# Optimization experiments

Hardware: AMD Instinct MI355X
Metric: run time of the kernel (lower is better)

Reference implementation:

```python
import jax, jax.numpy as jnp
import numpy as np

N_NODES = 50000
N_EDGES = 400000
F_DIM = 128        # num_embeddings
N_TYPES = 100      # num_atoms (embedding vocab)
CUTOFF = 5.0       # cutoff_dist
N_RBF = 20


def setup_inputs() -> dict:
    key = jax.random.key(0)
    ks = jax.random.split(key, 10)
    pos = jax.random.normal(ks[0], (N_NODES, 3), jnp.float32) * 3.0
    z = jax.random.randint(ks[1], (N_NODES,), 0, N_TYPES)
    edge_src = jax.random.randint(ks[2], (N_EDGES,), 0, N_NODES)
    edge_dst = jax.random.randint(ks[3], (N_EDGES,), 0, N_NODES)
    # avoid self-edges (rel_pos = 0 would make RBF sin(x)/x -> nan)
    edge_dst = jnp.where(edge_src == edge_dst, (edge_dst + 1) % N_NODES, edge_dst)
    eq = jnp.zeros((N_NODES, F_DIM, 3), jnp.float32)  # equivariant_repr init
    s = 1.0 / np.sqrt(F_DIM)
    emb_table = jax.random.normal(ks[4], (N_TYPES, F_DIM), jnp.float32) * s
    w_phi1 = jax.random.normal(ks[5], (F_DIM, F_DIM), jnp.float32) * s
    b_phi1 = jnp.zeros((F_DIM,), jnp.float32)
    w_phi2 = jax.random.normal(ks[6], (F_DIM, 3 * F_DIM), jnp.float32) * s
    b_phi2 = jnp.zeros((3 * F_DIM,), jnp.float32)
    w_rbf = jax.random.normal(ks[7], (N_RBF, 3 * F_DIM), jnp.float32) * (1.0 / np.sqrt(N_RBF))
    b_rbf = jnp.zeros((3 * F_DIM,), jnp.float32)
    return {"pos": pos, "eq": eq, "emb_table": emb_table,
            "w_phi1": w_phi1, "b_phi1": b_phi1,
            "w_phi2": w_phi2, "b_phi2": b_phi2,
            "w_rbf": w_rbf, "b_rbf": b_rbf,
            "z": z, "edge_src": edge_src, "edge_dst": edge_dst}


def reference(pos, eq, emb_table, w_phi1, b_phi1, w_phi2, b_phi2, w_rbf, b_rbf,
              z, edge_src, edge_dst):
    N = pos.shape[0]
    F_ = emb_table.shape[1]
    emb = emb_table[z]                                  # [N, F]
    # message pass over all edges (j = src neighbour, i = dst receiving node)
    rel = pos[edge_dst] - pos[edge_src]                 # pos[i] - pos[j], [E, 3]
    dist = jnp.linalg.norm(rel, axis=1)                 # [E]
    n = jnp.arange(1, N_RBF + 1, dtype=pos.dtype)       # [20]
    rbf = jnp.sin(n[None, :] * jnp.pi * dist[:, None] / CUTOFF) / dist[:, None]  # [E, 20]
    phi = jax.nn.silu(emb[edge_src] @ w_phi1 + b_phi1) @ w_phi2 + b_phi2          # [E, 3F]
    W = rbf @ w_rbf + b_rbf                             # [E, 3F]
    split = phi * W                                     # [E, 3F]
    d_emb = jax.ops.segment_sum(split[:, :F_], edge_dst, num_segments=N)          # [N, F]
    eq_msg = (eq[edge_src] * split[:, F_:2 * F_, None]
              + split[:, 2 * F_:, None] * rel[:, None, :] * dist[:, None, None])  # [E, F, 3]
    d_eq = jax.ops.segment_sum(eq_msg, edge_dst, num_segments=N)                  # [N, F, 3]
    return emb + d_emb, eq + d_eq
```

## Files before the change

### kernel.cpp

```cpp
#include <hip/hip_runtime.h>
#include <math.h>

#define N_NODES 50000
#define N_EDGES 400000
#define F_DIM   128
#define N_RBF   20
#define SCAN_B  256
#define N_CHUNK ((N_NODES + SCAN_B - 1) / SCAN_B)

__global__ void phi_table_kernel(const float* __restrict__ emb_table,
                                 const float* __restrict__ w_phi1,
                                 const float* __restrict__ b_phi1,
                                 const float* __restrict__ w_phi2,
                                 const float* __restrict__ b_phi2,
                                 float* __restrict__ phi_table) {
    __shared__ float emb_s[F_DIM];
    __shared__ float h_s[F_DIM];
    const int t = blockIdx.x;
    const int o = threadIdx.x;
    if (o < F_DIM) emb_s[o] = emb_table[t * F_DIM + o];
    __syncthreads();
    if (o < F_DIM) {
        float acc = b_phi1[o];
#pragma unroll 8
        for (int k = 0; k < F_DIM; ++k)
            acc = fmaf(emb_s[k], w_phi1[k * F_DIM + o], acc);
        h_s[o] = acc / (1.0f + expf(-acc));
    }
    __syncthreads();
    float a2 = b_phi2[o];
#pragma unroll 8
    for (int k = 0; k < F_DIM; ++k)
        a2 = fmaf(h_s[k], w_phi2[k * (3 * F_DIM) + o], a2);
    phi_table[t * (3 * F_DIM) + o] = a2;
}

__global__ void count_kernel(const int* __restrict__ edst, int* __restrict__ counts) {
    const int e = blockIdx.x * blockDim.x + threadIdx.x;
    if (e < N_EDGES) atomicAdd(&counts[edst[e]], 1);
}

__global__ void scan_partial_kernel(const int* __restrict__ counts,
                                    int* __restrict__ partial,
                                    int* __restrict__ chunk_sums) {
    __shared__ int s[SCAN_B];
    const int tid = threadIdx.x;
    const int gid = blockIdx.x * SCAN_B + tid;
    const int v = (gid < N_NODES) ? counts[gid] : 0;
    s[tid] = v;
    __syncthreads();
    for (int d = 1; d < SCAN_B; d <<= 1) {
        const int t = (tid >= d) ? s[tid - d] : 0;
        __syncthreads();
        s[tid] += t;
        __syncthreads();
    }
    if (gid < N_NODES) partial[gid] = s[tid] - v;
    if (tid == SCAN_B - 1) chunk_sums[blockIdx.x] = s[tid];
}

__global__ void scan_sums_kernel(int* __restrict__ chunk_sums,
                                 int* __restrict__ chunk_pref) {
    __shared__ int s[SCAN_B];
    const int tid = threadIdx.x;
    const int v = (tid < N_CHUNK) ? chunk_sums[tid] : 0;
    s[tid] = v;
    __syncthreads();
    for (int d = 1; d < SCAN_B; d <<= 1) {
        const int t = (tid >= d) ? s[tid - d] : 0;
        __syncthreads();
        s[tid] += t;
        __syncthreads();
    }
    if (tid < N_CHUNK) chunk_pref[tid] = s[tid] - v;
}

__global__ void finalize_offsets_kernel(const int* __restrict__ partial,
                                        const int* __restrict__ chunk_pref,
                                        int* __restrict__ offsets,
                                        int* __restrict__ cursor) {
    const int i = blockIdx.x * blockDim.x + threadIdx.x;
    if (i >= N_NODES) return;
    const int o = partial[i] + chunk_pref[i >> 8];
    offsets[i] = o;
    cursor[i]  = o;
}

__global__ void edge_pre_kernel(const float* __restrict__ pos,
                                const int* __restrict__ z,
                                const int* __restrict__ esrc,
                                const int* __restrict__ edst,
                                int* __restrict__ cursor,
                                float4* __restrict__ rec) {
    const int e = blockIdx.x * blockDim.x + threadIdx.x;
    if (e >= N_EDGES) return;
    const int j = esrc[e];
    const int i = edst[e];
    const int p = atomicAdd(&cursor[i], 1);

    const float px = pos[3 * i + 0] - pos[3 * j + 0];
    const float py = pos[3 * i + 1] - pos[3 * j + 1];
    const float pz = pos[3 * i + 2] - pos[3 * j + 2];
    const float d = sqrtf(px * px + py * py + pz * pz);
    const float inv_d = 1.0f / d;

    float sa, ca;
    sincosf(0.6283185307179586f * d, &sa, &ca);

    rec[2 * p] = make_float4(px, py, pz, d);
    float4 b;
    b.x = __int_as_float(j);
    b.y = __int_as_float(z[j]);
    b.z = sa * inv_d;
    b.w = 2.0f * ca;
    rec[2 * p + 1] = b;
}

__global__ void __launch_bounds__(256, 2)
gather_kernel(const float* __restrict__ eq,
              const float* __restrict__ emb_table,
              const float* __restrict__ phi_table,
              const float* __restrict__ w_rbf,
              const float* __restrict__ b_rbf,
              const int* __restrict__ z,
              const float4* __restrict__ rec,
              const int* __restrict__ offsets,
              const int* __restrict__ counts,
              float* __restrict__ out_emb,
              float* __restrict__ out_eq) {
    const int tid = threadIdx.x;
    const int grp = tid >> 7;
    const int f   = tid & 127;
    const int i   = blockIdx.x * 2 + grp;
    if (i >= N_NODES) return;

    const int start = offsets[i];
    const int cnt   = counts[i];

    float w1r[N_RBF], w2r[N_RBF], w3r[N_RBF];
#pragma unroll
    for (int n = 0; n < N_RBF; ++n) {
        const float* wr = w_rbf + n * (3 * F_DIM);
        w1r[n] = wr[f];
        w2r[n] = wr[F_DIM + f];
        w3r[n] = wr[2 * F_DIM + f];
    }
    const float br1 = b_rbf[f];
    const float br2 = b_rbf[F_DIM + f];
    const float br3 = b_rbf[2 * F_DIM + f];

    float accE = 0.f, ax = 0.f, ay = 0.f, az = 0.f;

    if (cnt > 0) {
        const int last = cnt - 1;
        const float* eqf = eq + (size_t)f * 3;
        const float* ptf = phi_table + f;

        float4 A0 = rec[2 * start];
        float4 B0 = rec[2 * start + 1];
        const int p1 = start + min(1, last);
        float4 A1 = rec[2 * p1];
        float4 B1 = rec[2 * p1 + 1];
        {
            const int j0 = __float_as_int(B0.x);
            const int t0 = __float_as_int(B0.y);
            const float* ej = eqf + (size_t)j0 * (F_DIM * 3);
            const float* pt = ptf + t0 * (3 * F_DIM);
            float e0 = ej[0], e1 = ej[1], e2 = ej[2];
            float p0 = pt[0], p1v = pt[F_DIM], p2v = pt[2 * F_DIM];

            float eq0 = e0, eq1 = e1, eq2 = e2;
            float ph0 = p0, ph1 = p1v, ph2 = p2v;

            for (int k = 0; k < cnt; ++k) {
                const int p2 = start + min(k + 2, last);
                const float4 A2 = rec[2 * p2];
                const float4 B2 = rec[2 * p2 + 1];

                const int j1 = __float_as_int(B1.x);
                const int t1 = __float_as_int(B1.y);
                const float* ej1 = eqf + (size_t)j1 * (F_DIM * 3);
                const float* pt1 = ptf + t1 * (3 * F_DIM);
                const float neq0 = ej1[0], neq1 = ej1[1], neq2 = ej1[2];
                const float nph0 = pt1[0], nph1 = pt1[F_DIM], nph2 = pt1[2 * F_DIM];

                float W1 = br1, W2 = br2, W3 = br3;
                float tm1 = 0.0f, tc = B0.z;
                const float twoc = B0.w;
#pragma unroll
                for (int n = 0; n < N_RBF; ++n) {
                    W1 = fmaf(tc, w1r[n], W1);
                    W2 = fmaf(tc, w2r[n], W2);
                    W3 = fmaf(tc, w3r[n], W3);
                    const float tn = fmaf(twoc, tc, -tm1);
                    tm1 = tc; tc = tn;
                }
                accE += ph0 * W1;
                const float s2 = ph1 * W2;
                const float s3 = ph2 * W3 * A0.w;
                ax = fmaf(eq0, s2, fmaf(s3, A0.x, ax));
                ay = fmaf(eq1, s2, fmaf(s3, A0.y, ay));
                az = fmaf(eq2, s2, fmaf(s3, A0.z, az));

                A0 = A1; B0 = B1; A1 = A2; B1 = B2;
                eq0 = neq0; eq1 = neq1; eq2 = neq2;
                ph0 = nph0; ph1 = nph1; ph2 = nph2;
            }
        }
    }

    out_emb[(size_t)i * F_DIM + f] = emb_table[z[i] * F_DIM + f] + accE;

    const float* ei = eq     + ((size_t)i * F_DIM + f) * 3;
    float*       od = out_eq + ((size_t)i * F_DIM + f) * 3;
    od[0] = ei[0] + ax;
    od[1] = ei[1] + ay;
    od[2] = ei[2] + az;
}

extern "C" void kernel_launch(void* const* d_in, const int* in_sizes, int n_in,
                              void* d_out, int out_size, void* d_ws, size_t ws_size,
                              hipStream_t stream) {
    const float* pos       = (const float*)d_in[0];
    const float* eq        = (const float*)d_in[1];
    const float* emb_table = (const float*)d_in[2];
    const float* w_phi1    = (const float*)d_in[3];
    const float* b_phi1    = (const float*)d_in[4];
    const float* w_phi2    = (const float*)d_in[5];
    const float* b_phi2    = (const float*)d_in[6];
    const float* w_rbf     = (const float*)d_in[7];
    const float* b_rbf     = (const float*)d_in[8];
    const int*   z         = (const int*)d_in[9];
    const int*   esrc      = (const int*)d_in[10];
    const int*   edst      = (const int*)d_in[11];

    float* out_emb = (float*)d_out;
    float* out_eq  = (float*)d_out + (size_t)N_NODES * F_DIM;

    char* ws = (char*)d_ws;
    float4* rec        = (float4*)ws;  ws += (size_t)N_EDGES * 32;
    float*  phi_table  = (float*)ws;   ws += 100 * 3 * F_DIM * 4;
    int*    counts     = (int*)ws;     ws += N_NODES * 4;
    int*    partial    = (int*)ws;     ws += N_NODES * 4;
    int*    offsets    = (int*)ws;     ws += N_NODES * 4;
    int*    cursor     = (int*)ws;     ws += N_NODES * 4;
    int*    chunk_sums = (int*)ws;     ws += SCAN_B * 4;
    int*    chunk_pref = (int*)ws;     ws += SCAN_B * 4;

    hipMemsetAsync(counts, 0, N_NODES * sizeof(int), stream);
    phi_table_kernel<<<100, 3 * F_DIM, 0, stream>>>(emb_table, w_phi1, b_phi1,
                                                    w_phi2, b_phi2, phi_table);
    count_kernel<<<(N_EDGES + 255) / 256, 256, 0, stream>>>(edst, counts);
    scan_partial_kernel<<<N_CHUNK, SCAN_B, 0, stream>>>(counts, partial, chunk_sums);
    scan_sums_kernel<<<1, SCAN_B, 0, stream>>>(chunk_sums, chunk_pref);
    finalize_offsets_kernel<<<(N_NODES + 255) / 256, 256, 0, stream>>>(
        partial, chunk_pref, offsets, cursor);
    edge_pre_kernel<<<(N_EDGES + 255) / 256, 256, 0, stream>>>(
        pos, z, esrc, edst, cursor, rec);
    gather_kernel<<<(N_NODES + 1) / 2, 256, 0, stream>>>(
        eq, emb_table, phi_table, w_rbf, b_rbf, z, rec,
        offsets, counts, out_emb, out_eq);
}
```

Baseline: 411.4 us.

## Process edges in chunks of four, streaming RBF weights instead of holding them in registers

The per-node gather loop now handles four edges per iteration. Each RBF weight triple is loaded once per chunk from memory (likely cache-resident) and reused across the four edges, instead of keeping all 60 weights in registers for the whole kernel. This frees registers, which should raise occupancy, and gives the four independent Chebyshev recurrences more instruction-level parallelism. The cost is reloading weights every chunk and computing masked padding edges when the degree is not a multiple of four; the prefetch of the next chunk's records replaces the old two-deep software pipeline.

```diff
diff --git a/kernel.cpp b/kernel.cpp
--- a/kernel.cpp
+++ b/kernel.cpp
@@ -5,6 +5,7 @@
 #define N_EDGES 400000
 #define F_DIM   128
 #define N_RBF   20
+#define EC      4
 #define SCAN_B  256
 #define N_CHUNK ((N_NODES + SCAN_B - 1) / SCAN_B)
 
@@ -137,75 +138,87 @@
     const int start = offsets[i];
     const int cnt   = counts[i];
 
-    float w1r[N_RBF], w2r[N_RBF], w3r[N_RBF];
-#pragma unroll
-    for (int n = 0; n < N_RBF; ++n) {
-        const float* wr = w_rbf + n * (3 * F_DIM);
-        w1r[n] = wr[f];
-        w2r[n] = wr[F_DIM + f];
-        w3r[n] = wr[2 * F_DIM + f];
-    }
     const float br1 = b_rbf[f];
     const float br2 = b_rbf[F_DIM + f];
     const float br3 = b_rbf[2 * F_DIM + f];
+    const float* wbase = w_rbf + f;
 
     float accE = 0.f, ax = 0.f, ay = 0.f, az = 0.f;
 
     if (cnt > 0) {
         const int last = cnt - 1;
-        const float* eqf = eq + (size_t)f * 3;
-        const float* ptf = phi_table + f;
-
-        float4 A0 = rec[2 * start];
-        float4 B0 = rec[2 * start + 1];
-        const int p1 = start + min(1, last);
-        float4 A1 = rec[2 * p1];
-        float4 B1 = rec[2 * p1 + 1];
-        {
-            const int j0 = __float_as_int(B0.x);
-            const int t0 = __float_as_int(B0.y);
-            const float* ej = eqf + (size_t)j0 * (F_DIM * 3);
-            const float* pt = ptf + t0 * (3 * F_DIM);
-            float e0 = ej[0], e1 = ej[1], e2 = ej[2];
-            float p0 = pt[0], p1v = pt[F_DIM], p2v = pt[2 * F_DIM];
-
-            float eq0 = e0, eq1 = e1, eq2 = e2;
-            float ph0 = p0, ph1 = p1v, ph2 = p2v;
-
-            for (int k = 0; k < cnt; ++k) {
-                const int p2 = start + min(k + 2, last);
-                const float4 A2 = rec[2 * p2];
-                const float4 B2 = rec[2 * p2 + 1];
-
-                const int j1 = __float_as_int(B1.x);
-                const int t1 = __float_as_int(B1.y);
-                const float* ej1 = eqf + (size_t)j1 * (F_DIM * 3);
-                const float* pt1 = ptf + t1 * (3 * F_DIM);
-                const float neq0 = ej1[0], neq1 = ej1[1], neq2 = ej1[2];
-                const float nph0 = pt1[0], nph1 = pt1[F_DIM], nph2 = pt1[2 * F_DIM];
-
-                float W1 = br1, W2 = br2, W3 = br3;
-                float tm1 = 0.0f, tc = B0.z;
-                const float twoc = B0.w;
-#pragma unroll
-                for (int n = 0; n < N_RBF; ++n) {
-                    W1 = fmaf(tc, w1r[n], W1);
-                    W2 = fmaf(tc, w2r[n], W2);
-                    W3 = fmaf(tc, w3r[n], W3);
-                    const float tn = fmaf(twoc, tc, -tm1);
-                    tm1 = tc; tc = tn;
+
+        float4 A[EC], Bv[EC];
+#pragma unroll
+        for (int s = 0; s < EC; ++s) {
+            const int p = start + min(s, last);
+            A[s]  = rec[2 * p];
+            Bv[s] = rec[2 * p + 1];
+        }
+
+        for (int base = 0; base < cnt; base += EC) {
+            float m[EC], tc[EC], tm1[EC], twoc[EC];
+            int   jj[EC], tt[EC];
+#pragma unroll
+            for (int s = 0; s < EC; ++s) {
+                m[s]    = (base + s < cnt) ? 1.0f : 0.0f;
+                jj[s]   = __float_as_int(Bv[s].x);
+                tt[s]   = __float_as_int(Bv[s].y);
+                tc[s]   = Bv[s].z;
+                tm1[s]  = 0.0f;
+                twoc[s] = Bv[s].w;
+            }
+
+            float eqv[EC][3], ph[EC][3];
+#pragma unroll
+            for (int s = 0; s < EC; ++s) {
+                const float* ej = eq + ((size_t)jj[s] * F_DIM + f) * 3;
+                eqv[s][0] = ej[0]; eqv[s][1] = ej[1]; eqv[s][2] = ej[2];
+                const float* pt = phi_table + tt[s] * (3 * F_DIM) + f;
+                ph[s][0] = pt[0]; ph[s][1] = pt[F_DIM]; ph[s][2] = pt[2 * F_DIM];
+            }
+
+            float4 An[EC], Bn[EC];
+#pragma unroll
+            for (int s = 0; s < EC; ++s) {
+                const int p = start + min(base + EC + s, last);
+                An[s] = rec[2 * p];
+                Bn[s] = rec[2 * p + 1];
+            }
+
+            float W1[EC], W2[EC], W3[EC];
+#pragma unroll
+            for (int s = 0; s < EC; ++s) { W1[s] = br1; W2[s] = br2; W3[s] = br3; }
+#pragma unroll
+            for (int n = 0; n < N_RBF; ++n) {
+                const float w1 = wbase[n * (3 * F_DIM)];
+                const float w2 = wbase[n * (3 * F_DIM) + F_DIM];
+                const float w3 = wbase[n * (3 * F_DIM) + 2 * F_DIM];
+#pragma unroll
+                for (int s = 0; s < EC; ++s) {
+                    W1[s] = fmaf(tc[s], w1, W1[s]);
+                    W2[s] = fmaf(tc[s], w2, W2[s]);
+                    W3[s] = fmaf(tc[s], w3, W3[s]);
+                    const float tn = fmaf(twoc[s], tc[s], -tm1[s]);
+                    tm1[s] = tc[s]; tc[s] = tn;
                 }
-                accE += ph0 * W1;
-                const float s2 = ph1 * W2;
-                const float s3 = ph2 * W3 * A0.w;
-                ax = fmaf(eq0, s2, fmaf(s3, A0.x, ax));
-                ay = fmaf(eq1, s2, fmaf(s3, A0.y, ay));
-                az = fmaf(eq2, s2, fmaf(s3, A0.z, az));
-
-                A0 = A1; B0 = B1; A1 = A2; B1 = B2;
-                eq0 = neq0; eq1 = neq1; eq2 = neq2;
-                ph0 = nph0; ph1 = nph1; ph2 = nph2;
-            }
+            }
+
+#pragma unroll
+            for (int s = 0; s < EC; ++s) {
+                const float p0 = m[s] * ph[s][0];
+                const float p1 = m[s] * ph[s][1];
+                const float p2 = m[s] * ph[s][2];
+                accE = fmaf(p0, W1[s], accE);
+                const float s2 = p1 * W2[s];
+                const float s3 = p2 * W3[s] * A[s].w;
+                ax = fmaf(eqv[s][0], s2, fmaf(s3, A[s].x, ax));
+                ay = fmaf(eqv[s][1], s2, fmaf(s3, A[s].y, ay));
+                az = fmaf(eqv[s][2], s2, fmaf(s3, A[s].z, az));
+            }
+
+#pragma unroll
+            for (int s = 0; s < EC; ++s) { A[s] = An[s]; Bv[s] = Bn[s]; }
         }
     }
 
```

Result: slower. 441.7 us (+7.4%).

## Process two edges per iteration with packed float2 FMAs and streamed RBF weights

Applied to the files above, without the earlier changes.

Restructures the per-node edge loop to handle two edges per iteration. The Chebyshev RBF recurrence and weight FMAs run on two-wide float vectors so the compiler can emit packed FP32 FMA instructions. The 60 register-resident RBF weights are dropped and the weights are reloaded from memory inside the loop, which lowers register pressure but adds repeated cached loads. The odd tail edge is masked to zero through its phi values, and the software prefetch of eq/phi one iteration ahead is removed.

```diff
diff --git a/kernel.cpp b/kernel.cpp
--- a/kernel.cpp
+++ b/kernel.cpp
@@ -7,6 +7,8 @@
 #define N_RBF   20
 #define SCAN_B  256
 #define N_CHUNK ((N_NODES + SCAN_B - 1) / SCAN_B)
+
+typedef float f2 __attribute__((ext_vector_type(2)));
 
 __global__ void phi_table_kernel(const float* __restrict__ emb_table,
                                  const float* __restrict__ w_phi1,
@@ -137,75 +139,83 @@
     const int start = offsets[i];
     const int cnt   = counts[i];
 
-    float w1r[N_RBF], w2r[N_RBF], w3r[N_RBF];
-#pragma unroll
-    for (int n = 0; n < N_RBF; ++n) {
-        const float* wr = w_rbf + n * (3 * F_DIM);
-        w1r[n] = wr[f];
-        w2r[n] = wr[F_DIM + f];
-        w3r[n] = wr[2 * F_DIM + f];
-    }
     const float br1 = b_rbf[f];
     const float br2 = b_rbf[F_DIM + f];
     const float br3 = b_rbf[2 * F_DIM + f];
+    const float* wbase = w_rbf + f;
 
     float accE = 0.f, ax = 0.f, ay = 0.f, az = 0.f;
 
     if (cnt > 0) {
         const int last = cnt - 1;
-        const float* eqf = eq + (size_t)f * 3;
-        const float* ptf = phi_table + f;
 
         float4 A0 = rec[2 * start];
         float4 B0 = rec[2 * start + 1];
         const int p1 = start + min(1, last);
         float4 A1 = rec[2 * p1];
         float4 B1 = rec[2 * p1 + 1];
-        {
-            const int j0 = __float_as_int(B0.x);
-            const int t0 = __float_as_int(B0.y);
-            const float* ej = eqf + (size_t)j0 * (F_DIM * 3);
-            const float* pt = ptf + t0 * (3 * F_DIM);
-            float e0 = ej[0], e1 = ej[1], e2 = ej[2];
-            float p0 = pt[0], p1v = pt[F_DIM], p2v = pt[2 * F_DIM];
-
-            float eq0 = e0, eq1 = e1, eq2 = e2;
-            float ph0 = p0, ph1 = p1v, ph2 = p2v;
-
-            for (int k = 0; k < cnt; ++k) {
-                const int p2 = start + min(k + 2, last);
-                const float4 A2 = rec[2 * p2];
-                const float4 B2 = rec[2 * p2 + 1];
-
-                const int j1 = __float_as_int(B1.x);
-                const int t1 = __float_as_int(B1.y);
-                const float* ej1 = eqf + (size_t)j1 * (F_DIM * 3);
-                const float* pt1 = ptf + t1 * (3 * F_DIM);
-                const float neq0 = ej1[0], neq1 = ej1[1], neq2 = ej1[2];
-                const float nph0 = pt1[0], nph1 = pt1[F_DIM], nph2 = pt1[2 * F_DIM];
-
-                float W1 = br1, W2 = br2, W3 = br3;
-                float tm1 = 0.0f, tc = B0.z;
-                const float twoc = B0.w;
+
+        for (int base = 0; base < cnt; base += 2) {
+            const int pn0 = start + min(base + 2, last);
+            const int pn1 = start + min(base + 3, last);
+            const float4 A2 = rec[2 * pn0];
+            const float4 B2 = rec[2 * pn0 + 1];
+            const float4 A3 = rec[2 * pn1];
+            const float4 B3 = rec[2 * pn1 + 1];
+
+            const int ja = __float_as_int(B0.x), ta = __float_as_int(B0.y);
+            const int jb = __float_as_int(B1.x), tb = __float_as_int(B1.y);
+            const float* eja = eq + ((size_t)ja * F_DIM + f) * 3;
+            const float* ejb = eq + ((size_t)jb * F_DIM + f) * 3;
+            const float eqa0 = eja[0], eqa1 = eja[1], eqa2 = eja[2];
+            const float eqb0 = ejb[0], eqb1 = ejb[1], eqb2 = ejb[2];
+            const float* pta = phi_table + ta * (3 * F_DIM) + f;
+            const float* ptb = phi_table + tb * (3 * F_DIM) + f;
+            const float pha0 = pta[0], pha1 = pta[F_DIM], pha2 = pta[2 * F_DIM];
+            const float mb = (base + 1 < cnt) ? 1.0f : 0.0f;
+            const float phb0 = mb * ptb[0];
+            const float phb1 = mb * ptb[F_DIM];
+            const float phb2 = mb * ptb[2 * F_DIM];
+
+            f2 W1 = {br1, br1};
+            f2 W2 = {br2, br2};
+            f2 W3 = {br3, br3};
+            f2 tc   = {B0.z, B1.z};
+            f2 twoc = {B0.w, B1.w};
+            f2 tm1  = {0.0f, 0.0f};
 #pragma unroll
-                for (int n = 0; n < N_RBF; ++n) {
-                    W1 = fmaf(tc, w1r[n], W1);
-                    W2 = fmaf(tc, w2r[n], W2);
-                    W3 = fmaf(tc, w3r[n], W3);
-                    const float tn = fmaf(twoc, tc, -tm1);
-                    tm1 = tc; tc = tn;
-                }
-                accE += ph0 * W1;
-                const float s2 = ph1 * W2;
-                const float s3 = ph2 * W3 * A0.w;
-                ax = fmaf(eq0, s2, fmaf(s3, A0.x, ax));
-                ay = fmaf(eq1, s2, fmaf(s3, A0.y, ay));
-                az = fmaf(eq2, s2, fmaf(s3, A0.z, az));
-
-                A0 = A1; B0 = B1; A1 = A2; B1 = B2;
-                eq0 = neq0; eq1 = neq1; eq2 = neq2;
-                ph0 = nph0; ph1 = nph1; ph2 = nph2;
+            for (int n = 0; n < N_RBF; ++n) {
+                const float w1 = wbase[n * (3 * F_DIM)];
+                const float w2 = wbase[n * (3 * F_DIM) + F_DIM];
+                const float w3 = wbase[n * (3 * F_DIM) + 2 * F_DIM];
+                const f2 w1v = {w1, w1};
+                const f2 w2v = {w2, w2};
+                const f2 w3v = {w3, w3};
+                W1 = __builtin_elementwise_fma(tc, w1v, W1);
+                W2 = __builtin_elementwise_fma(tc, w2v, W2);
+                W3 = __builtin_elementwise_fma(tc, w3v, W3);
+                const f2 tn = __builtin_elementwise_fma(twoc, tc, -tm1);
+                tm1 = tc; tc = tn;
             }
+
+            accE = fmaf(pha0, W1.x, accE);
+            {
+                const float s2 = pha1 * W2.x;
+                const float s3 = pha2 * W3.x * A0.w;
+                ax = fmaf(eqa0, s2, fmaf(s3, A0.x, ax));
+                ay = fmaf(eqa1, s2, fmaf(s3, A0.y, ay));
+                az = fmaf(eqa2, s2, fmaf(s3, A0.z, az));
+            }
+            accE = fmaf(phb0, W1.y, accE);
+            {
+                const float s2 = phb1 * W2.y;
+                const float s3 = phb2 * W3.y * A1.w;
+                ax = fmaf(eqb0, s2, fmaf(s3, A1.x, ax));
+                ay = fmaf(eqb1, s2, fmaf(s3, A1.y, ay));
+                az = fmaf(eqb2, s2, fmaf(s3, A1.z, az));
+            }
+
+            A0 = A2; B0 = B2; A1 = A3; B1 = B3;
         }
     }
 
```

New measurement: 585.5 us. 42.3% more time.
